# Kernel tuning notes

Measured on AMD Instinct MI355X. Metric: run time of the kernel, lower is better.

Reference implementation:

```python
import jax, jax.numpy as jnp
import numpy as np

HIDDEN_DIM = 2048
NUM_HEADS = 16
HEAD_DIM = HIDDEN_DIM // NUM_HEADS


def setup_inputs() -> dict:
    key = jax.random.key(0)
    ks = jax.random.split(key, 5)
    B, S, D = 2, 2048, HIDDEN_DIM
    scale = 1.0 / np.sqrt(D)
    return {
        "x": jax.random.normal(ks[0], (B, S, D), dtype=jnp.float32),
        "w_q": jax.random.normal(ks[1], (D, D), dtype=jnp.float32) * scale,
        "w_k": jax.random.normal(ks[2], (D, D), dtype=jnp.float32) * scale,
        "w_v": jax.random.normal(ks[3], (D, D), dtype=jnp.float32) * scale,
        "w_o": jax.random.normal(ks[4], (D, D), dtype=jnp.float32) * scale,
        "causal": 1,
    }


def _attention(q, k, v, causal):
    # q,k,v: (B, S, D) -> split heads -> (B, H, S, d)
    B, S, D = q.shape
    q = q.reshape(B, S, NUM_HEADS, HEAD_DIM).transpose(0, 2, 1, 3)
    k = k.reshape(B, S, NUM_HEADS, HEAD_DIM).transpose(0, 2, 1, 3)
    v = v.reshape(B, S, NUM_HEADS, HEAD_DIM).transpose(0, 2, 1, 3)
    scale = 1.0 / np.sqrt(HEAD_DIM)
    # scores: (B, H, S, S)
    s = jnp.einsum("bhqd,bhkd->bhqk", q, k) * scale
    if causal:
        qpos = jnp.arange(S)[:, None]
        kpos = jnp.arange(S)[None, :]
        s = jnp.where(kpos > qpos, -jnp.inf, s)
    # stable softmax; rows that are fully -inf cannot occur with causal mask
    p = jax.nn.softmax(s, axis=-1)
    o = jnp.einsum("bhqk,bhkd->bhqd", p, v)
    return o.transpose(0, 2, 1, 3).reshape(B, S, D)


def reference(x, w_q, w_k, w_v, w_o, causal):
    q = x @ w_q.T
    k = x @ w_k.T
    v = x @ w_v.T
    o = _attention(q, k, v, bool(causal))
    return o @ w_o.T
```

## Files before the change

kernel.cpp:

```cpp
#include <hip/hip_runtime.h>


typedef __attribute__((ext_vector_type(8))) short short8;
typedef __attribute__((ext_vector_type(4))) short bfs4;
typedef __attribute__((ext_vector_type(4))) float floatx4;

__device__ __forceinline__ void gl_lds16(const void* g, void* l) {
  __builtin_amdgcn_global_load_lds((const __attribute__((address_space(1))) void*)g,
                                   (__attribute__((address_space(3))) void*)l, 16, 0, 0);
}

__device__ __forceinline__ short f2bf(float f) {
  union { float f; unsigned u; } a; a.f = f;
  unsigned r = a.u + 0x7FFFu + ((a.u >> 16) & 1u);
  return (short)(r >> 16);
}

__global__ __launch_bounds__(256) void cvt_bf16(
    const float* __restrict__ s0, const float* __restrict__ s1,
    const float* __restrict__ s2, const float* __restrict__ s3,
    const float* __restrict__ s4,
    short* __restrict__ d0, short* __restrict__ d1, short* __restrict__ d2,
    short* __restrict__ d3, short* __restrict__ d4,
    int n0, int nw) {
  const int z = blockIdx.z;
  const float* s = (z == 0) ? s0 : (z == 1) ? s1 : (z == 2) ? s2 : (z == 3) ? s3 : s4;
  short* d      = (z == 0) ? d0 : (z == 1) ? d1 : (z == 2) ? d2 : (z == 3) ? d3 : d4;
  const int n   = (z == 0) ? n0 : nw;
  const int stride = gridDim.x * blockDim.x * 4;
  for (int i = (blockIdx.x * blockDim.x + threadIdx.x) * 4; i < n; i += stride) {
    float4 v = *(const float4*)(s + i);
    bfs4 o;
    o[0] = f2bf(v.x); o[1] = f2bf(v.y); o[2] = f2bf(v.z); o[3] = f2bf(v.w);
    *(bfs4*)(d + i) = o;
  }
}

__global__ __launch_bounds__(256, 2) void gemm_bt(
    const short* __restrict__ A,
    const short* __restrict__ B0, const short* __restrict__ B1, const short* __restrict__ B2,
    short* __restrict__ C0, short* __restrict__ C1, short* __restrict__ C2,
    int M, int N, int K) {
  const short* Bm = (blockIdx.z == 0) ? B0 : ((blockIdx.z == 1) ? B1 : B2);
  short* C = (blockIdx.z == 0) ? C0 : ((blockIdx.z == 1) ? C1 : C2);

  __shared__ short As[128 * 64];
  __shared__ short Bs[128 * 64];

  const int tid = threadIdx.x;
  const int w = tid >> 6, l = tid & 63;
  const int lane15 = l & 15, quad = l >> 4;
  const int wr = w >> 1, wc = w & 1;
  const int row0 = blockIdx.y * 128;
  const int col0 = blockIdx.x * 128;

  floatx4 acc[4][4] = {};
  const int srow = l >> 3;
  const int sg = l & 7;

  for (int k0 = 0; k0 < K; k0 += 64) {
#pragma unroll
    for (int j = 0; j < 4; ++j) {
      int chunk = j * 4 + w;
      int row = chunk * 8 + srow;
      int g = sg ^ (row & 7);
      gl_lds16(A  + (size_t)(row0 + row) * K + k0 + g * 8, &As[chunk * 512]);
      gl_lds16(Bm + (size_t)(col0 + row) * K + k0 + g * 8, &Bs[chunk * 512]);
    }
    __syncthreads();
#pragma unroll
    for (int ks = 0; ks < 2; ++ks) {
      short8 af[4], bf[4];
#pragma unroll
      for (int i = 0; i < 4; ++i) {
        int rowA = wr * 64 + i * 16 + lane15;
        af[i] = *(const short8*)&As[rowA * 64 + (((ks * 4 + quad) ^ (rowA & 7)) << 3)];
        int rowB = wc * 64 + i * 16 + lane15;
        bf[i] = *(const short8*)&Bs[rowB * 64 + (((ks * 4 + quad) ^ (rowB & 7)) << 3)];
      }
#pragma unroll
      for (int i = 0; i < 4; ++i)
#pragma unroll
        for (int jj = 0; jj < 4; ++jj)
          acc[i][jj] = __builtin_amdgcn_mfma_f32_16x16x32_bf16(af[i], bf[jj], acc[i][jj], 0, 0, 0);
    }
    __syncthreads();
  }

#pragma unroll
  for (int i = 0; i < 4; ++i)
#pragma unroll
    for (int jj = 0; jj < 4; ++jj)
#pragma unroll
      for (int r = 0; r < 4; ++r) {
        int row = row0 + wr * 64 + i * 16 + quad * 4 + r;
        int col = col0 + wc * 64 + jj * 16 + lane15;
        C[(size_t)row * N + col] = f2bf(acc[i][jj][r]);
      }
}

__global__ __launch_bounds__(256, 2) void gemm_bt_f32out(
    const short* __restrict__ A, const short* __restrict__ Bm,
    float* __restrict__ C, int M, int N, int K) {
  __shared__ short As[128 * 64];
  __shared__ short Bs[128 * 64];

  const int tid = threadIdx.x;
  const int w = tid >> 6, l = tid & 63;
  const int lane15 = l & 15, quad = l >> 4;
  const int wr = w >> 1, wc = w & 1;
  const int row0 = blockIdx.y * 128;
  const int col0 = blockIdx.x * 128;

  floatx4 acc[4][4] = {};
  const int srow = l >> 3;
  const int sg = l & 7;

  for (int k0 = 0; k0 < K; k0 += 64) {
#pragma unroll
    for (int j = 0; j < 4; ++j) {
      int chunk = j * 4 + w;
      int row = chunk * 8 + srow;
      int g = sg ^ (row & 7);
      gl_lds16(A  + (size_t)(row0 + row) * K + k0 + g * 8, &As[chunk * 512]);
      gl_lds16(Bm + (size_t)(col0 + row) * K + k0 + g * 8, &Bs[chunk * 512]);
    }
    __syncthreads();
#pragma unroll
    for (int ks = 0; ks < 2; ++ks) {
      short8 af[4], bf[4];
#pragma unroll
      for (int i = 0; i < 4; ++i) {
        int rowA = wr * 64 + i * 16 + lane15;
        af[i] = *(const short8*)&As[rowA * 64 + (((ks * 4 + quad) ^ (rowA & 7)) << 3)];
        int rowB = wc * 64 + i * 16 + lane15;
        bf[i] = *(const short8*)&Bs[rowB * 64 + (((ks * 4 + quad) ^ (rowB & 7)) << 3)];
      }
#pragma unroll
      for (int i = 0; i < 4; ++i)
#pragma unroll
        for (int jj = 0; jj < 4; ++jj)
          acc[i][jj] = __builtin_amdgcn_mfma_f32_16x16x32_bf16(af[i], bf[jj], acc[i][jj], 0, 0, 0);
    }
    __syncthreads();
  }

#pragma unroll
  for (int i = 0; i < 4; ++i)
#pragma unroll
    for (int jj = 0; jj < 4; ++jj)
#pragma unroll
      for (int r = 0; r < 4; ++r) {
        int row = row0 + wr * 64 + i * 16 + quad * 4 + r;
        int col = col0 + wc * 64 + jj * 16 + lane15;
        C[(size_t)row * N + col] = acc[i][jj][r];
      }
}

__global__ __launch_bounds__(512, 4) void attn_fused(
    const short* __restrict__ Qg, const short* __restrict__ Kg,
    const short* __restrict__ Vg, short* __restrict__ Og,
    const int* __restrict__ causal_p) {
  constexpr int S = 2048, D = 2048, HDim = 128;
  constexpr int PS = 40;
  __shared__ __align__(16) short smem[38144];
  short* Ps  = smem + 32768;
  float* aLds = (float*)(smem + 37888);
  short* Qs  = smem;
  floatx4* F4 = (floatx4*)smem;

  const int tid = threadIdx.x;
  const int w = tid >> 6, l = tid & 63;
  const int lane15 = l & 15, quad = l >> 4;
  const int w4 = w & 3, grp = w >> 2;
  const int bh = blockIdx.y, b = bh >> 4, h = bh & 15;
  const size_t rbase = (size_t)b * S;
  const int c0 = h * HDim;
  const int causal = *causal_p;
  short* Pw = Ps + w * (16 * PS);
  constexpr float SCL = 0.08838834764831845f * 1.4426950408889634f;

  const int vt8 = tid & 255, vtile = tid >> 8;
  const int vs = vt8 & 31, vdg = vt8 >> 5;
  const int sg8 = vs >> 3, so = vs & 7;

  const int krow = w * 4 + quad;
  const int kgs = lane15 ^ (krow & 7);

#pragma unroll 1
  for (int ph = 0; ph < 2; ++ph) {
    const int jt = ph ? (31 - blockIdx.x) : blockIdx.x;
    const int q0 = jt * 64;
    const int wrow0 = q0 + w4 * 16;

#pragma unroll
    for (int j = 0; j < 2; ++j) {
      int row = j * 32 + w * 4 + quad;
      int gs = lane15 ^ (row & 7);
      gl_lds16(Qg + (rbase + q0 + row) * D + c0 + gs * 8, &Qs[(j * 8 + w) * 512]);
    }
    __syncthreads();
    short8 qf[4];
#pragma unroll
    for (int ks = 0; ks < 4; ++ks) {
      int row = w4 * 16 + lane15;
      qf[ks] = *(const short8*)&Qs[row * HDim + (((ks * 4 + quad) ^ (row & 7)) << 3)];
    }
    __syncthreads();

    floatx4 ot[8] = {};
    float psum[4] = {0.f, 0.f, 0.f, 0.f};
    const int ktiles = causal ? (q0 / 32 + 2) : (S / 32);
    const int iters = ktiles >> 1;

    short* Kcur = smem;
    short* Knxt = smem + 8192;
    short* Vcur = smem + 16384;
    short* Vnxt = smem + 24576;

    gl_lds16(Kg + (rbase + krow) * D + c0 + kgs * 8, &Kcur[w * 512]);
    gl_lds16(Kg + (rbase + 32 + krow) * D + c0 + kgs * 8, &Kcur[4096 + w * 512]);
    {
      const short* vp = Vg + (rbase + vtile * 32 + vs) * D + c0 + vdg * 16;
      short8 v0 = *(const short8*)vp;
      short8 v1 = *(const short8*)(vp + 8);
      short* Vtb = Vcur + vtile * 4096;
#pragma unroll
      for (int e = 0; e < 8; ++e) {
        int d0 = vdg * 16 + e, d1 = vdg * 16 + 8 + e;
        Vtb[d0 * 32 + ((sg8 ^ (d0 & 3)) << 3) + so] = v0[e];
        Vtb[d1 * 32 + ((sg8 ^ (d1 & 3)) << 3) + so] = v1[e];
      }
    }
    __syncthreads();

    for (int it = 0; it < iters; ++it) {
      const int k0A = it * 64;
      const bool pf = (it + 1 < iters);
      short8 pv0, pv1;
      if (pf) {
        const int k0N = k0A + 64;
        gl_lds16(Kg + (rbase + k0N + krow) * D + c0 + kgs * 8, &Knxt[w * 512]);
        gl_lds16(Kg + (rbase + k0N + 32 + krow) * D + c0 + kgs * 8, &Knxt[4096 + w * 512]);
        const short* vp = Vg + (rbase + k0N + vtile * 32 + vs) * D + c0 + vdg * 16;
        pv0 = *(const short8*)vp;
        pv1 = *(const short8*)(vp + 8);
      }

      const int k0 = k0A + grp * 32;
      const short* Kc = Kcur + grp * 4096;
      const short* Vc = Vcur + grp * 4096;
      if (!causal || k0 <= wrow0 + 15) {
        floatx4 sacc[2] = {};
#pragma unroll
        for (int ks = 0; ks < 4; ++ks) {
          short8 kf0, kf1;
          {
            int row = lane15;
            kf0 = *(const short8*)&Kc[row * HDim + (((ks * 4 + quad) ^ (row & 7)) << 3)];
            row = 16 + lane15;
            kf1 = *(const short8*)&Kc[row * HDim + (((ks * 4 + quad) ^ (row & 7)) << 3)];
          }
          sacc[0] = __builtin_amdgcn_mfma_f32_16x16x32_bf16(qf[ks], kf0, sacc[0], 0, 0, 0);
          sacc[1] = __builtin_amdgcn_mfma_f32_16x16x32_bf16(qf[ks], kf1, sacc[1], 0, 0, 0);
        }
#pragma unroll
        for (int r = 0; r < 4; ++r) {
          int prow = quad * 4 + r;
          int qrow = wrow0 + prow;
          float s0 = fminf(sacc[0][r] * SCL, 115.0f);
          float s1 = fminf(sacc[1][r] * SCL, 115.0f);
          float p0 = exp2f(s0);
          float p1 = exp2f(s1);
          if (causal) {
            if (k0 + lane15 > qrow)      p0 = 0.f;
            if (k0 + 16 + lane15 > qrow) p1 = 0.f;
          }
          psum[r] += p0 + p1;
          Pw[prow * PS + lane15]      = f2bf(p0);
          Pw[prow * PS + 16 + lane15] = f2bf(p1);
        }
        short8 pfr = *(const short8*)&Pw[lane15 * PS + quad * 8];
#pragma unroll
        for (int cd = 0; cd < 8; ++cd) {
          int d = cd * 16 + lane15;
          short8 vf = *(const short8*)&Vc[d * 32 + ((quad ^ (d & 3)) << 3)];
          ot[cd] = __builtin_amdgcn_mfma_f32_16x16x32_bf16(vf, pfr, ot[cd], 0, 0, 0);
        }
      }

      if (pf) {
        short* Vtb = Vnxt + vtile * 4096;
#pragma unroll
        for (int e = 0; e < 8; ++e) {
          int d0 = vdg * 16 + e, d1 = vdg * 16 + 8 + e;
          Vtb[d0 * 32 + ((sg8 ^ (d0 & 3)) << 3) + so] = pv0[e];
          Vtb[d1 * 32 + ((sg8 ^ (d1 & 3)) << 3) + so] = pv1[e];
        }
      }
      __syncthreads();
      short* t = Kcur; Kcur = Knxt; Knxt = t;
      t = Vcur; Vcur = Vnxt; Vnxt = t;
    }

#pragma unroll
    for (int r = 0; r < 4; ++r) {
      float s = psum[r];
      s += __shfl_xor(s, 1, 64);
      s += __shfl_xor(s, 2, 64);
      s += __shfl_xor(s, 4, 64);
      s += __shfl_xor(s, 8, 64);
      if (lane15 == 0) aLds[grp * 64 + w4 * 16 + quad * 4 + r] = s;
    }
    if (grp == 1) {
      int qrow = w4 * 16 + lane15;
#pragma unroll
      for (int cd = 0; cd < 8; ++cd)
        F4[qrow * 32 + ((cd * 4 + quad) ^ ((qrow & 7) << 2))] = ot[cd];
    }
    __syncthreads();
    float invq = 0.f;
    if (grp == 0) {
      int qrow = w4 * 16 + lane15;
      invq = 1.0f / (aLds[qrow] + aLds[64 + qrow]);
#pragma unroll
      for (int cd = 0; cd < 8; ++cd) {
        floatx4 o2 = F4[qrow * 32 + ((cd * 4 + quad) ^ ((qrow & 7) << 2))];
        ot[cd] += o2;
      }
    }
    __syncthreads();
    if (grp == 0) {
      int qrow = w4 * 16 + lane15;
#pragma unroll
      for (int cd = 0; cd < 8; ++cd)
#pragma unroll
        for (int r = 0; r < 4; ++r) {
          int col = cd * 16 + quad * 4 + r;
          Qs[qrow * HDim + (((col >> 3) ^ (qrow & 7)) << 3) + (col & 7)] =
              f2bf(ot[cd][r] * invq);
        }
    }
    __syncthreads();
#pragma unroll
    for (int i = 0; i < 2; ++i) {
      int c = i * 512 + tid;
      int row = c >> 4, g = c & 15;
      *(short8*)(Og + (rbase + q0 + row) * D + c0 + g * 8) =
          *(const short8*)&Qs[row * HDim + ((g ^ (row & 7)) << 3)];
    }
    __syncthreads();
  }
}

extern "C" void kernel_launch(void* const* d_in, const int* in_sizes, int n_in,
                              void* d_out, int out_size, void* d_ws, size_t ws_size,
                              hipStream_t stream) {
  const float* x  = (const float*)d_in[0];
  const float* wq = (const float*)d_in[1];
  const float* wk = (const float*)d_in[2];
  const float* wv = (const float*)d_in[3];
  const float* wo = (const float*)d_in[4];
  const int* causal = (const int*)d_in[5];
  float* out = (float*)d_out;

  const int M = 4096, N = 2048, K = 2048;
  const int NX = M * K;
  const int NW = N * K;

  char* ws = (char*)d_ws;
  short* xb  = (short*)(ws);
  short* wqb = (short*)(ws + 16u * 1024 * 1024);
  short* wkb = (short*)(ws + 24u * 1024 * 1024);
  short* wvb = (short*)(ws + 32u * 1024 * 1024);
  short* wob = (short*)(ws + 40u * 1024 * 1024);
  short* q   = (short*)(ws + 48u * 1024 * 1024);
  short* k   = (short*)(ws + 64u * 1024 * 1024);
  short* v   = (short*)(ws + 80u * 1024 * 1024);
  short* o   = (short*)(ws + 96u * 1024 * 1024);

  dim3 blk(256);
  cvt_bf16<<<dim3(2048, 1, 5), blk, 0, stream>>>(x, wq, wk, wv, wo,
                                                 xb, wqb, wkb, wvb, wob, NX, NW);
  gemm_bt<<<dim3(N / 128, M / 128, 3), blk, 0, stream>>>(xb, wqb, wkb, wvb,
                                                         q, k, v, M, N, K);
  attn_fused<<<dim3(16, 32), dim3(512), 0, stream>>>(q, k, v, o, causal);
  gemm_bt_f32out<<<dim3(N / 128, M / 128, 1), blk, 0, stream>>>(o, wob, out, M, N, K);
}
```

Baseline: 389.1 us.

## Load V directly into LDS and read it with transpose-read instructions

Replaces the register-staged, scalar-scattered transposed store of V into LDS with direct global-to-LDS 16-byte loads in row-major layout, matching the K path. The PV MFMA operand is then fetched with ds_read_b64_tr_b16 transpose reads instead of swizzled short8 loads. This removes per-iteration VGPR staging and many 2-byte LDS writes, freeing registers and LDS bandwidth. In exchange it relies on inline asm with an explicit lgkmcnt wait and a sched barrier, and the unswizzled V layout may cause LDS bank conflicts.

Result: no change. 392.6 us (+0.9%).

```diff
diff --git a/kernel.cpp b/kernel.cpp
--- a/kernel.cpp
+++ b/kernel.cpp
@@ -180,12 +180,10 @@
   short* Pw = Ps + w * (16 * PS);
   constexpr float SCL = 0.08838834764831845f * 1.4426950408889634f;
 
-  const int vt8 = tid & 255, vtile = tid >> 8;
-  const int vs = vt8 & 31, vdg = vt8 >> 5;
-  const int sg8 = vs >> 3, so = vs & 7;
-
   const int krow = w * 4 + quad;
   const int kgs = lane15 ^ (krow & 7);
+  const int vrow = l >> 1;
+  const int vcol = w * 16 + (l & 1) * 8;
 
 #pragma unroll 1
   for (int ph = 0; ph < 2; ++ph) {
@@ -220,31 +218,19 @@
 
     gl_lds16(Kg + (rbase + krow) * D + c0 + kgs * 8, &Kcur[w * 512]);
     gl_lds16(Kg + (rbase + 32 + krow) * D + c0 + kgs * 8, &Kcur[4096 + w * 512]);
-    {
-      const short* vp = Vg + (rbase + vtile * 32 + vs) * D + c0 + vdg * 16;
-      short8 v0 = *(const short8*)vp;
-      short8 v1 = *(const short8*)(vp + 8);
-      short* Vtb = Vcur + vtile * 4096;
-#pragma unroll
-      for (int e = 0; e < 8; ++e) {
-        int d0 = vdg * 16 + e, d1 = vdg * 16 + 8 + e;
-        Vtb[d0 * 32 + ((sg8 ^ (d0 & 3)) << 3) + so] = v0[e];
-        Vtb[d1 * 32 + ((sg8 ^ (d1 & 3)) << 3) + so] = v1[e];
-      }
-    }
+    gl_lds16(Vg + (rbase + vrow) * D + c0 + vcol, &Vcur[w * 512]);
+    gl_lds16(Vg + (rbase + 32 + vrow) * D + c0 + vcol, &Vcur[4096 + w * 512]);
     __syncthreads();
 
     for (int it = 0; it < iters; ++it) {
       const int k0A = it * 64;
       const bool pf = (it + 1 < iters);
-      short8 pv0, pv1;
       if (pf) {
         const int k0N = k0A + 64;
         gl_lds16(Kg + (rbase + k0N + krow) * D + c0 + kgs * 8, &Knxt[w * 512]);
         gl_lds16(Kg + (rbase + k0N + 32 + krow) * D + c0 + kgs * 8, &Knxt[4096 + w * 512]);
-        const short* vp = Vg + (rbase + k0N + vtile * 32 + vs) * D + c0 + vdg * 16;
-        pv0 = *(const short8*)vp;
-        pv1 = *(const short8*)(vp + 8);
+        gl_lds16(Vg + (rbase + k0N + vrow) * D + c0 + vcol, &Vnxt[w * 512]);
+        gl_lds16(Vg + (rbase + k0N + 32 + vrow) * D + c0 + vcol, &Vnxt[4096 + w * 512]);
       }
 
       const int k0 = k0A + grp * 32;
@@ -281,23 +267,24 @@
           Pw[prow * PS + 16 + lane15] = f2bf(p1);
         }
         short8 pfr = *(const short8*)&Pw[lane15 * PS + quad * 8];
+        const unsigned vbase = (unsigned)(size_t)Vc + (quad << 8) + (lane15 << 3);
+        bfs4 vlo[8], vhi[8];
+#pragma unroll
+        for (int cd = 0; cd < 8; ++cd)
+          asm volatile("ds_read_b64_tr_b16 %0, %2\n\t"
+                       "ds_read_b64_tr_b16 %1, %2 offset:128"
+                       : "=&v"(vlo[cd]), "=&v"(vhi[cd])
+                       : "v"(vbase + (cd << 10)));
+        asm volatile("s_waitcnt lgkmcnt(0)" ::: "memory");
+        __builtin_amdgcn_sched_barrier(0);
 #pragma unroll
         for (int cd = 0; cd < 8; ++cd) {
-          int d = cd * 16 + lane15;
-          short8 vf = *(const short8*)&Vc[d * 32 + ((quad ^ (d & 3)) << 3)];
+          short8 vf = {vlo[cd][0], vlo[cd][1], vlo[cd][2], vlo[cd][3],
+                       vhi[cd][0], vhi[cd][1], vhi[cd][2], vhi[cd][3]};
           ot[cd] = __builtin_amdgcn_mfma_f32_16x16x32_bf16(vf, pfr, ot[cd], 0, 0, 0);
         }
       }
 
-      if (pf) {
-        short* Vtb = Vnxt + vtile * 4096;
-#pragma unroll
-        for (int e = 0; e < 8; ++e) {
-          int d0 = vdg * 16 + e, d1 = vdg * 16 + 8 + e;
-          Vtb[d0 * 32 + ((sg8 ^ (d0 & 3)) << 3) + so] = pv0[e];
-          Vtb[d1 * 32 + ((sg8 ^ (d1 & 3)) << 3) + so] = pv1[e];
-        }
-      }
       __syncthreads();
       short* t = Kcur; Kcur = Knxt; Knxt = t;
       t = Vcur; Vcur = Vnxt; Vnxt = t;
```
